# Kernel tuning notes

Measured on AMD Instinct MI355X. Metric: run time of the kernel, lower is better.

Reference implementation:

```python
import jax, jax.numpy as jnp
import numpy as np

B, S, QD = 1, 2048, 3072          # batch, seq, query_dim
H, D = 24, 128                    # heads, head_dim
INNER = H * D                     # 3072
MLP = 4 * QD                      # mlp_hidden_dim = 12288
EPS = 1e-5


def setup_inputs() -> dict:
    key = jax.random.key(0)
    k0, k1, k2 = jax.random.split(key, 3)
    hidden_states = jax.random.normal(k0, (B, S, QD), dtype=jnp.float32)
    # RoPE tables (non-neox / interleaved), [S, D/2]
    pos = jnp.arange(S, dtype=jnp.float32)
    inv_freq = 1.0 / (10000.0 ** (jnp.arange(0, D, 2, dtype=jnp.float32) / D))
    ang = pos[:, None] * inv_freq[None, :]
    cos, sin = jnp.cos(ang), jnp.sin(ang)
    # learned params
    W_qkv_mlp = jax.random.normal(k1, (QD, 3 * INNER + 2 * MLP), dtype=jnp.float32) * 0.02
    norm_q_w = jnp.ones((D,), dtype=jnp.float32)
    norm_k_w = jnp.ones((D,), dtype=jnp.float32)
    W_out = jax.random.normal(k2, (INNER + MLP, QD), dtype=jnp.float32) * 0.02
    b_out = jnp.zeros((QD,), dtype=jnp.float32)
    return {"hidden_states": hidden_states, "cos": cos, "sin": sin,
            "W_qkv_mlp": W_qkv_mlp, "norm_q_w": norm_q_w, "norm_k_w": norm_k_w,
            "W_out": W_out, "b_out": b_out}


def _rmsnorm(x, w, eps):
    return x * jax.lax.rsqrt(jnp.mean(x * x, axis=-1, keepdims=True) + eps) * w


def _rope_interleaved(x, cos, sin):
    # x: [B,S,H,D]; cos/sin: [S,D/2]; non-neox pairing (x[2i], x[2i+1]); fp32 math
    xf = x.astype(jnp.float32)
    x1, x2 = xf[..., 0::2], xf[..., 1::2]
    c = cos[None, :, None, :]
    s = sin[None, :, None, :]
    r1 = x1 * c - x2 * s
    r2 = x2 * c + x1 * s
    out = jnp.stack([r1, r2], axis=-1).reshape(x.shape)
    return out.astype(x.dtype)


def reference(hidden_states, cos, sin, W_qkv_mlp, norm_q_w, norm_k_w, W_out, b_out):
    # fused QKV + MLP input projection (no bias)
    h = hidden_states @ W_qkv_mlp                       # [B,S,3*INNER+2*MLP]
    qkv, mlp_hidden = jnp.split(h, [3 * INNER], axis=-1)
    q, k, v = jnp.split(qkv, 3, axis=-1)
    q = q.reshape(B, S, H, D)
    k = k.reshape(B, S, H, D)
    v = v.reshape(B, S, H, D)
    # per-head RMSNorm on q/k
    q = _rmsnorm(q, norm_q_w, EPS)
    k = _rmsnorm(k, norm_k_w, EPS)
    # interleaved RoPE
    q = _rope_interleaved(q, cos, sin)
    k = _rope_interleaved(k, cos, sin)
    # non-causal attention, scale = 1/sqrt(head_dim)
    scale = 1.0 / np.sqrt(D).astype(np.float32)
    scores = jnp.einsum('bqhd,bkhd->bhqk', q, k) * scale
    probs = jax.nn.softmax(scores, axis=-1)
    attn_out = jnp.einsum('bhqk,bkhd->bqhd', probs, v).reshape(B, S, INNER)
    # SwiGLU on fused MLP hidden (gate fused into first GEMM)
    x1, x2 = jnp.split(mlp_hidden, 2, axis=-1)
    mlp_out = jax.nn.silu(x1) * x2                      # [B,S,MLP]
    # fused output projection (with bias)
    return jnp.concatenate([attn_out, mlp_out], axis=-1) @ W_out + b_out
```

## Files before the change

kernel.cpp:

```cpp
#include <hip/hip_runtime.h>

typedef unsigned short u16;
typedef unsigned int u32;
typedef __attribute__((ext_vector_type(8))) __bf16 bf16x8;
typedef __attribute__((ext_vector_type(4))) float f32x4;
typedef __attribute__((ext_vector_type(8))) u16 u16x8;
typedef __attribute__((ext_vector_type(4))) float fv4;

#define DEVI __device__ __forceinline__

DEVI float bf2f(u16 u) { union { u32 i; float f; } v; v.i = ((u32)u) << 16; return v.f; }
DEVI u16 f2bf(float f) {
  union { float f; u32 i; } v; v.f = f;
  u32 r = v.i + 0x7fffu + ((v.i >> 16) & 1u);
  return (u16)(r >> 16);
}

#define GLD16(src, dst)                                                        \
  __builtin_amdgcn_global_load_lds(                                            \
      (const __attribute__((address_space(1))) void*)(src),                    \
      (__attribute__((address_space(3))) void*)(dst), 16, 0, 0)

DEVI f32x4 mfma16(bf16x8 a, bf16x8 b, f32x4 c) {
  return __builtin_amdgcn_mfma_f32_16x16x32_bf16(a, b, c, 0, 0, 0);
}

constexpr int S_    = 2048;
constexpr int QD_   = 3072;
constexpr int H_    = 24;
constexpr int N1_   = 33792;
constexpr int K1_   = 3072;
constexpr int K2_   = 15360;
constexpr int N2_   = 3072;
constexpr int MLP_  = 12288;

__global__ void k_cvt(const float* __restrict__ in, u16* __restrict__ out) {
  int i = blockIdx.x * blockDim.x + threadIdx.x;
  const fv4* p = (const fv4*)in + (size_t)i * 2;
  fv4 a = p[0], b = p[1];
  u16x8 r;
#pragma unroll
  for (int e = 0; e < 4; ++e) { r[e] = f2bf(a[e]); r[4 + e] = f2bf(b[e]); }
  ((u16x8*)out)[i] = r;
}

__global__ __launch_bounds__(256)
void k_tconv(const float* __restrict__ in, u16* __restrict__ out, int R, int C) {
  __shared__ u16 tile[64][80];
  const int t = threadIdx.x;
  const int r0 = blockIdx.y * 64, c0 = blockIdx.x * 64;
  {
    const int rl = t >> 2, cc = t & 3;
    const float* src = in + (size_t)(r0 + rl) * C + c0 + cc * 16;
    fv4 v0 = *(const fv4*)(src), v1 = *(const fv4*)(src + 4);
    fv4 v2 = *(const fv4*)(src + 8), v3 = *(const fv4*)(src + 12);
    u16x8 u0, u1;
#pragma unroll
    for (int e = 0; e < 4; ++e) {
      u0[e] = f2bf(v0[e]); u0[4 + e] = f2bf(v1[e]);
      u1[e] = f2bf(v2[e]); u1[4 + e] = f2bf(v3[e]);
    }
    *(u16x8*)&tile[rl][cc * 16] = u0;
    *(u16x8*)&tile[rl][cc * 16 + 8] = u1;
  }
  __syncthreads();
  {
    const int cl = t >> 2, rc = t & 3;
    u16x8 u0, u1;
#pragma unroll
    for (int j = 0; j < 8; ++j) {
      u0[j] = tile[rc * 16 + j][cl];
      u1[j] = tile[rc * 16 + 8 + j][cl];
    }
    u16* dst = out + (size_t)(c0 + cl) * R + r0 + rc * 16;
    *(u16x8*)dst = u0;
    *(u16x8*)(dst + 8) = u1;
  }
}

template <int BM, int BN, int WM, int WN, bool OUTF32>
__global__ __launch_bounds__(256)
void k_gemm(const u16* __restrict__ A, const u16* __restrict__ Bt,
            void* __restrict__ Cout, const float* __restrict__ bias,
            int M, int N, int K) {
  constexpr int FM = WM / 16, FN = WN / 16;
  constexpr int WNC = BN / WN;
  __shared__ u16 As[BM * 32];
  __shared__ u16 Bs[BN * 32];
  const int t = threadIdx.x, w = t >> 6, lane = t & 63;
  const int m0 = blockIdx.x * BM, n0 = blockIdx.y * BN;
  const int wr = w / WNC, wc = w % WNC;
  const int g = lane >> 4, rr = lane & 15;
  const int sm = lane >> 2, sk = (lane & 3) * 8;
  f32x4 acc[FM][FN] = {};
  const int nk = K >> 5;
  for (int kt = 0; kt < nk; ++kt) {
    __syncthreads();
    const int kb = kt * 32 + sk;
#pragma unroll
    for (int c = 0; c < BM / 64; ++c) {
      const int ch = w + c * 4;
      GLD16(A + (size_t)(m0 + ch * 16 + sm) * K + kb, &As[ch * 512]);
    }
#pragma unroll
    for (int c = 0; c < BN / 64; ++c) {
      const int ch = w + c * 4;
      GLD16(Bt + (size_t)(n0 + ch * 16 + sm) * K + kb, &Bs[ch * 512]);
    }
    __syncthreads();
    bf16x8 af[FM], bfr[FN];
#pragma unroll
    for (int mi = 0; mi < FM; ++mi)
      af[mi] = *reinterpret_cast<const bf16x8*>(&As[(wr * WM + mi * 16 + rr) * 32 + g * 8]);
#pragma unroll
    for (int ni = 0; ni < FN; ++ni)
      bfr[ni] = *reinterpret_cast<const bf16x8*>(&Bs[(wc * WN + ni * 16 + rr) * 32 + g * 8]);
#pragma unroll
    for (int mi = 0; mi < FM; ++mi)
#pragma unroll
      for (int ni = 0; ni < FN; ++ni)
        acc[mi][ni] = mfma16(af[mi], bfr[ni], acc[mi][ni]);
  }
#pragma unroll
  for (int mi = 0; mi < FM; ++mi)
#pragma unroll
    for (int ni = 0; ni < FN; ++ni) {
      const int row = m0 + wr * WM + mi * 16 + g * 4;
      const int col = n0 + wc * WN + ni * 16 + rr;
#pragma unroll
      for (int j = 0; j < 4; ++j) {
        if constexpr (OUTF32)
          ((float*)Cout)[(size_t)(row + j) * N + col] = acc[mi][ni][j] + bias[col];
        else
          ((u16*)Cout)[(size_t)(row + j) * N + col] = f2bf(acc[mi][ni][j]);
      }
    }
}

#define BARX() asm volatile("s_barrier" ::: "memory")
__global__ __launch_bounds__(512, 2)
void k_gemm256(const u16* __restrict__ A, const u16* __restrict__ Bt,
               u16* __restrict__ C, int N, int K, int nbm) {
  extern __shared__ char smem[];
  const int t = threadIdx.x;
  const int w = t >> 6, lane = t & 63;
  const int wr = w >> 2, wc = w & 3, bh = wc >> 1;
  const int g = lane >> 4, rr = lane & 15;
  const int nwg = gridDim.x, bid = blockIdx.x;
  const int swz = (bid & 7) * (nwg >> 3) + (bid >> 3);
  const int m0 = (swz % nbm) * 256;
  const int n0 = (swz / nbm) * 256;
  const int o = t * 16;
  const int ou = o ^ (((o >> 9) & 1) << 5);
  const int srow = ((ou >> 10) >> 1) * 16 + ((ou >> 6) & 15);
  const int scol = ((ou >> 10) & 1) * 32 + ((ou & 63) >> 1);
  const int soff = (rr * 64 + g * 16) ^ (((rr >> 3) & 1) << 5);
  const int bnoff = (wc & 1) * 8192;
  const int nk = K >> 6;

  const u16* Arow = A + (size_t)(m0 + srow) * K + scol;
  const u16* Brow = Bt + (size_t)(n0 + srow) * K + scol;
#define LDSA(buf, h) (smem + ((buf) * 2 + (h)) * 16384 + w * 1024)
#define LDSB(buf, h) (smem + 65536 + ((buf) * 2 + (h)) * 16384 + w * 1024)
#define STG(rowptr, h, k0, dst)                                   \
  do {                                                            \
    const u16* _s = (rowptr) + (size_t)(h) * 128 * K + (k0);      \
    GLD16(_s, (dst));                                             \
    GLD16(_s + (size_t)64 * K, (dst) + 8192);                     \
  } while (0)

  STG(Arow, 0, 0, LDSA(0, 0));
  STG(Arow, 1, 0, LDSA(0, 1));
  STG(Brow, 0, 0, LDSB(0, 0));
  STG(Brow, 1, 0, LDSB(0, 1));
  STG(Brow, 0, 64, LDSB(1, 0));
  STG(Brow, 1, 64, LDSB(1, 1));
  STG(Arow, 0, 64, LDSA(1, 0));
  asm volatile("s_waitcnt vmcnt(6)" ::: "memory");
  BARX();

  f32x4 acc[8][4] = {};
  for (int j = 0; j < nk; ++j) {
    const int b = j & 1;
    const char* Ab = smem + ((b << 1) + wr) * 16384;
    const char* Bb = smem + 65536 + ((b << 1) + bh) * 16384;
    const int jb = (j + 2 < nk) ? j + 2 : nk - 1;
    bf16x8 aL[4][2], aH[4][2], bL[2][2], bH[2][2];
#pragma unroll
    for (int m = 0; m < 4; ++m)
#pragma unroll
      for (int kk = 0; kk < 2; ++kk)
        aL[m][kk] = *(const bf16x8*)(Ab + m * 2048 + kk * 1024 + soff);
#pragma unroll
    for (int n = 0; n < 2; ++n)
#pragma unroll
      for (int kk = 0; kk < 2; ++kk)
        bL[n][kk] = *(const bf16x8*)(Bb + bnoff + n * 2048 + kk * 1024 + soff);
    if (j + 1 < nk) STG(Arow, 1, (j + 1) * 64, LDSA((j + 1) & 1, 1));
    BARX();
    __builtin_amdgcn_s_setprio(1);
#pragma unroll
    for (int m = 0; m < 4; ++m)
#pragma unroll
      for (int n = 0; n < 2; ++n)
#pragma unroll
        for (int kk = 0; kk < 2; ++kk)
          acc[m][n] = mfma16(aL[m][kk], bL[n][kk], acc[m][n]);
    __builtin_amdgcn_s_setprio(0);
    BARX();
#pragma unroll
    for (int n = 0; n < 2; ++n)
#pragma unroll
      for (int kk = 0; kk < 2; ++kk)
        bH[n][kk] = *(const bf16x8*)(Bb + bnoff + (n + 2) * 2048 + kk * 1024 + soff);
    BARX();
    __builtin_amdgcn_s_setprio(1);
#pragma unroll
    for (int m = 0; m < 4; ++m)
#pragma unroll
      for (int n = 0; n < 2; ++n)
#pragma unroll
        for (int kk = 0; kk < 2; ++kk)
          acc[m][n + 2] = mfma16(aL[m][kk], bH[n][kk], acc[m][n + 2]);
    __builtin_amdgcn_s_setprio(0);
    BARX();
#pragma unroll
    for (int m = 0; m < 4; ++m)
#pragma unroll
      for (int kk = 0; kk < 2; ++kk)
        aH[m][kk] = *(const bf16x8*)(Ab + (m + 4) * 2048 + kk * 1024 + soff);
    STG(Brow, 0, jb * 64, LDSB(b, 0));
    BARX();
    __builtin_amdgcn_s_setprio(1);
#pragma unroll
    for (int m = 0; m < 4; ++m)
#pragma unroll
      for (int n = 0; n < 2; ++n)
#pragma unroll
        for (int kk = 0; kk < 2; ++kk)
          acc[m + 4][n] = mfma16(aH[m][kk], bL[n][kk], acc[m + 4][n]);
    __builtin_amdgcn_s_setprio(0);
    BARX();
    STG(Brow, 1, jb * 64, LDSB(b, 1));
    STG(Arow, 0, jb * 64, LDSA(b, 0));
    asm volatile("s_waitcnt vmcnt(6)" ::: "memory");
    BARX();
    __builtin_amdgcn_s_setprio(1);
#pragma unroll
    for (int m = 0; m < 4; ++m)
#pragma unroll
      for (int n = 0; n < 2; ++n)
#pragma unroll
        for (int kk = 0; kk < 2; ++kk)
          acc[m + 4][n + 2] = mfma16(aH[m][kk], bH[n][kk], acc[m + 4][n + 2]);
    __builtin_amdgcn_s_setprio(0);
    BARX();
  }
#pragma unroll
  for (int m = 0; m < 8; ++m)
#pragma unroll
    for (int n = 0; n < 4; ++n) {
      const int row = m0 + wr * 128 + m * 16 + g * 4;
      const int col = n0 + wc * 64 + n * 16 + rr;
#pragma unroll
      for (int jj = 0; jj < 4; ++jj)
        C[(size_t)(row + jj) * N + col] = f2bf(acc[m][n][jj]);
    }
#undef LDSA
#undef LDSB
#undef STG
}

__global__ __launch_bounds__(256)
void k_qknr(u16* __restrict__ h, const float* __restrict__ cosT,
            const float* __restrict__ sinT, const float* __restrict__ wq,
            const float* __restrict__ wk) {
  const int row = blockIdx.x * 4 + (threadIdx.x >> 6);
  const int lane = threadIdx.x & 63;
  const int s = row / 48;
  const int r2 = row - s * 48;
  const int qk = r2 / 24;
  const int head = r2 - qk * 24;
  u16* base = h + (size_t)s * N1_ + qk * 3072 + head * 128;
  u32 pv = *(const u32*)(base + 2 * lane);
  float x1 = bf2f((u16)(pv & 0xffff)), x2 = bf2f((u16)(pv >> 16));
  float ss = x1 * x1 + x2 * x2;
#pragma unroll
  for (int off = 32; off >= 1; off >>= 1) ss += __shfl_xor(ss, off);
  const float inv = rsqrtf(ss * (1.0f / 128.0f) + 1e-5f);
  const float* wv = qk ? wk : wq;
  const float w1 = wv[2 * lane], w2 = wv[2 * lane + 1];
  const float c = cosT[s * 64 + lane], sn = sinT[s * 64 + lane];
  float xn1 = x1 * inv * w1, xn2 = x2 * inv * w2;
  float r1 = xn1 * c - xn2 * sn;
  float r2v = xn2 * c + xn1 * sn;
  if (!qk) { r1 *= 0.08838834764831845f; r2v *= 0.08838834764831845f; }
  *(u32*)(base + 2 * lane) = (u32)f2bf(r1) | ((u32)f2bf(r2v) << 16);
}

__global__ __launch_bounds__(256)
void k_vt(const u16* __restrict__ h, u16* __restrict__ vt) {
  __shared__ u16 tile[64][144];
  const int t = threadIdx.x;
  const int head = blockIdx.y;
  const int s0 = blockIdx.x * 64;
  {
    const int sl = t >> 2, cc = t & 3;
    const u16* src = h + (size_t)(s0 + sl) * N1_ + 6144 + head * 128 + cc * 32;
#pragma unroll
    for (int q = 0; q < 4; ++q)
      *(u16x8*)&tile[sl][cc * 32 + q * 8] = *(const u16x8*)(src + q * 8);
  }
  __syncthreads();
  {
    const int d = t & 127, half = t >> 7;
    u16* dst = vt + ((size_t)head * 128 + d) * S_ + s0 + half * 32;
#pragma unroll
    for (int q = 0; q < 4; ++q) {
      u16x8 v;
#pragma unroll
      for (int e = 0; e < 8; ++e) v[e] = tile[half * 32 + q * 8 + e][d];
      *(u16x8*)(dst + q * 8) = v;
    }
  }
}

__global__ __launch_bounds__(256)
void k_attn(const u16* __restrict__ h, const u16* __restrict__ vt,
            u16* __restrict__ cc) {
  extern __shared__ char smem[];
  char* KsB = smem;
  char* VsB = smem + 32768;
  const int t = threadIdx.x, w = t >> 6, lane = t & 63;
  const int g = lane >> 4, c = lane & 15;
  u16* Pw = (u16*)(smem + 65536 + w * 2304);
  const int head = blockIdx.y;
  const int q0 = blockIdx.x * 64 + w * 16;
  const int wb = w * 1024;

  const u16* ksrc[4];
  const u16* vsrc[4];
#pragma unroll
  for (int p = 0; p < 4; ++p) {
    const int o = p * 4096 + wb + lane * 16;
    {
      const int kc = o >> 12, r = (o >> 6) & 63, db = o & 63;
      ksrc[p] = h + (size_t)r * N1_ + 3072 + head * 128 + kc * 32 + db / 2;
    }
    {
      const int ks = o >> 13, d = (o >> 6) & 127, db = o & 63;
      vsrc[p] = vt + (size_t)(head * 128 + d) * S_ + ks * 32 + db / 2;
    }
  }
#define STAGEA(ts, buf)                                                     \
  do {                                                                      \
    const size_t _ka = (size_t)(ts) * 64 * N1_;                             \
    const int _kv = (ts) * 64;                                              \
    _Pragma("unroll") for (int p = 0; p < 4; ++p)                           \
        GLD16(ksrc[p] + _ka, KsB + (buf) * 16384 + p * 4096 + wb);          \
    _Pragma("unroll") for (int p = 0; p < 4; ++p)                           \
        GLD16(vsrc[p] + _kv, VsB + (buf) * 16384 + p * 4096 + wb);          \
  } while (0)

  bf16x8 aq[4];
  {
    const u16* qr = h + (size_t)(q0 + c) * N1_ + head * 128;
#pragma unroll
    for (int kc = 0; kc < 4; ++kc)
      aq[kc] = *reinterpret_cast<const bf16x8*>(qr + kc * 32 + g * 8);
  }
  f32x4 o[8] = {};
  float m_[4] = {-1e30f, -1e30f, -1e30f, -1e30f};
  float l_[4] = {0.f, 0.f, 0.f, 0.f};

  STAGEA(0, 0);
  STAGEA(1, 1);
  asm volatile("s_waitcnt vmcnt(8)" ::: "memory");
  __builtin_amdgcn_s_barrier();

  for (int tt = 0; tt < 32; ++tt) {
    const int buf = tt & 1;
    const char* Kb = KsB + buf * 16384;
    const char* Vb = VsB + buf * 16384;
    f32x4 sc[4] = {};
    __builtin_amdgcn_s_setprio(1);
#pragma unroll
    for (int nf = 0; nf < 4; ++nf)
#pragma unroll
      for (int kc = 0; kc < 4; ++kc) {
        bf16x8 bk = *(const bf16x8*)(Kb + kc * 4096 + (nf * 16 + c) * 64 + g * 16);
        sc[nf] = mfma16(aq[kc], bk, sc[nf]);
      }
    __builtin_amdgcn_s_setprio(0);
    float rmax[4];
#pragma unroll
    for (int j = 0; j < 4; ++j)
      rmax[j] = fmaxf(fmaxf(sc[0][j], sc[1][j]), fmaxf(sc[2][j], sc[3][j]));
#pragma unroll
    for (int j = 0; j < 4; ++j)
#pragma unroll
      for (int off = 8; off >= 1; off >>= 1)
        rmax[j] = fmaxf(rmax[j], __shfl_xor(rmax[j], off));
    float al[4], rs[4];
#pragma unroll
    for (int j = 0; j < 4; ++j) {
      const float mn = fmaxf(m_[j], rmax[j]);
      al[j] = __expf(m_[j] - mn);
      m_[j] = mn;
      rs[j] = 0.f;
    }
#pragma unroll
    for (int nf = 0; nf < 4; ++nf)
#pragma unroll
      for (int j = 0; j < 4; ++j) {
        const float pr = __expf(sc[nf][j] - m_[j]);
        sc[nf][j] = pr;
        rs[j] += pr;
      }
#pragma unroll
    for (int j = 0; j < 4; ++j) {
#pragma unroll
      for (int off = 8; off >= 1; off >>= 1) rs[j] += __shfl_xor(rs[j], off);
      l_[j] = l_[j] * al[j] + rs[j];
    }
#pragma unroll
    for (int of = 0; of < 8; ++of)
#pragma unroll
      for (int j = 0; j < 4; ++j) o[of][j] *= al[j];
#pragma unroll
    for (int nf = 0; nf < 4; ++nf)
#pragma unroll
      for (int j = 0; j < 4; ++j)
        Pw[(g * 4 + j) * 72 + nf * 16 + c] = f2bf(sc[nf][j]);
    asm volatile("s_waitcnt lgkmcnt(0)" ::: "memory");
    bf16x8 ap[2];
#pragma unroll
    for (int ks = 0; ks < 2; ++ks)
      ap[ks] = *(const bf16x8*)(Pw + c * 72 + ks * 32 + g * 8);
    __builtin_amdgcn_s_setprio(1);
#pragma unroll
    for (int of = 0; of < 8; ++of)
#pragma unroll
      for (int ks = 0; ks < 2; ++ks) {
        bf16x8 bv = *(const bf16x8*)(Vb + ks * 8192 + (of * 16 + c) * 64 + g * 16);
        o[of] = mfma16(ap[ks], bv, o[of]);
      }
    __builtin_amdgcn_s_setprio(0);
    __builtin_amdgcn_s_barrier();
    const int tn = (tt + 2 < 32) ? tt + 2 : 31;
    STAGEA(tn, buf);
    asm volatile("s_waitcnt vmcnt(8)" ::: "memory");
    __builtin_amdgcn_s_barrier();
  }
  float inv[4];
#pragma unroll
  for (int j = 0; j < 4; ++j) inv[j] = 1.0f / l_[j];
#pragma unroll
  for (int of = 0; of < 8; ++of)
#pragma unroll
    for (int j = 0; j < 4; ++j)
      cc[(size_t)(q0 + g * 4 + j) * K2_ + head * 128 + of * 16 + c] =
          f2bf(o[of][j] * inv[j]);
#undef STAGEA
}

__global__ void k_mlpact(const u16* __restrict__ h, u16* __restrict__ cc) {
  const int i = blockIdx.x * blockDim.x + threadIdx.x;
  const int s = i / 1536;
  const int j8 = i - s * 1536;
  const u16x8 a8 = *((const u16x8*)(h + (size_t)s * N1_ + 9216) + j8);
  const u16x8 b8 = *((const u16x8*)(h + (size_t)s * N1_ + 21504) + j8);
  u16x8 r;
#pragma unroll
  for (int e = 0; e < 8; ++e) {
    float a = bf2f(a8[e]), b = bf2f(b8[e]);
    float sv = a / (1.0f + expf(-a));
    r[e] = f2bf(sv * b);
  }
  *((u16x8*)(cc + (size_t)s * K2_ + 3072) + j8) = r;
}

extern "C" void kernel_launch(void* const* d_in, const int* in_sizes, int n_in,
                              void* d_out, int out_size, void* d_ws,
                              size_t ws_size, hipStream_t stream) {
  const float* hs   = (const float*)d_in[0];
  const float* cosT = (const float*)d_in[1];
  const float* sinT = (const float*)d_in[2];
  const float* W1   = (const float*)d_in[3];
  const float* wq   = (const float*)d_in[4];
  const float* wk   = (const float*)d_in[5];
  const float* W2   = (const float*)d_in[6];
  const float* bo   = (const float*)d_in[7];
  float* out = (float*)d_out;

  char* p = (char*)d_ws;
  u16* Abf  = (u16*)p; p += (size_t)S_ * K1_ * 2;
  u16* W1t  = (u16*)p; p += (size_t)N1_ * K1_ * 2;
  u16* W2t  = (u16*)p; p += (size_t)N2_ * K2_ * 2;
  u16* Hbuf = (u16*)p; p += (size_t)S_ * N1_ * 2;
  u16* Vt   = (u16*)p; p += (size_t)H_ * 128 * S_ * 2;
  u16* CC   = (u16*)p; p += (size_t)S_ * K2_ * 2;
  if ((size_t)(p - (char*)d_ws) > ws_size) return;

  k_cvt<<<(S_ * K1_) / (256 * 8), 256, 0, stream>>>(hs, Abf);
  k_tconv<<<dim3(N1_ / 64, K1_ / 64), 256, 0, stream>>>(W1, W1t, K1_, N1_);
  k_tconv<<<dim3(N2_ / 64, K2_ / 64), 256, 0, stream>>>(W2, W2t, K2_, N2_);

  hipError_t aerr = hipFuncSetAttribute(
      reinterpret_cast<const void*>(k_gemm256),
      hipFuncAttributeMaxDynamicSharedMemorySize, 131072);
  if (aerr == hipSuccess) {
    k_gemm256<<<dim3(1056), 512, 131072, stream>>>(Abf, W1t, Hbuf,
                                                   N1_, K1_, 8);
  } else {
    k_gemm<128, 128, 64, 64, false>
        <<<dim3(S_ / 128, N1_ / 128), 256, 0, stream>>>(Abf, W1t, Hbuf, nullptr,
                                                        S_, N1_, K1_);
  }
  k_qknr<<<(S_ * 2 * H_) / 4, 256, 0, stream>>>(Hbuf, cosT, sinT, wq, wk);
  k_vt<<<dim3(S_ / 64, H_), 256, 0, stream>>>(Hbuf, Vt);
  (void)hipFuncSetAttribute(reinterpret_cast<const void*>(k_attn),
                            hipFuncAttributeMaxDynamicSharedMemorySize, 75776);
  k_attn<<<dim3(S_ / 64, H_), 256, 75776, stream>>>(Hbuf, Vt, CC);
  k_mlpact<<<(S_ * MLP_) / (256 * 8), 256, 0, stream>>>(Hbuf, CC);
  k_gemm<128, 128, 64, 64, true>
      <<<dim3(S_ / 128, N2_ / 128), 256, 0, stream>>>(CC, W2t, out, bo,
                                                      S_, N2_, K2_);
}
```

Before: 1.223 ms.

## Transpose weights via register 8x8 blocks and add explicit LDS waitcnts in GEMM

Replaces the LDS-tiled fp32-to-bf16 weight transpose with a register-only version in which each thread loads an 8x8 fp32 block and writes eight 16-byte bf16 rows, with 128x128 tiles per block. This removes the shared-memory staging and barrier and widens the output writes. The global reads become strided 32-byte row segments, which may coalesce less well. The main GEMM also gets explicit lgkmcnt waits around its barriers, so the LDS fragment loads partly overlap the barrier instead of relying on compiler-inserted waits.

```diff
diff --git a/kernel.cpp b/kernel.cpp
--- a/kernel.cpp
+++ b/kernel.cpp
@@ -45,36 +45,27 @@
 }
 
 __global__ __launch_bounds__(256)
-void k_tconv(const float* __restrict__ in, u16* __restrict__ out, int R, int C) {
-  __shared__ u16 tile[64][80];
+void k_tconv8(const float* __restrict__ in, u16* __restrict__ out,
+              int R, int C) {
   const int t = threadIdx.x;
-  const int r0 = blockIdx.y * 64, c0 = blockIdx.x * 64;
-  {
-    const int rl = t >> 2, cc = t & 3;
-    const float* src = in + (size_t)(r0 + rl) * C + c0 + cc * 16;
-    fv4 v0 = *(const fv4*)(src), v1 = *(const fv4*)(src + 4);
-    fv4 v2 = *(const fv4*)(src + 8), v3 = *(const fv4*)(src + 12);
-    u16x8 u0, u1;
-#pragma unroll
-    for (int e = 0; e < 4; ++e) {
-      u0[e] = f2bf(v0[e]); u0[4 + e] = f2bf(v1[e]);
-      u1[e] = f2bf(v2[e]); u1[4 + e] = f2bf(v3[e]);
-    }
-    *(u16x8*)&tile[rl][cc * 16] = u0;
-    *(u16x8*)&tile[rl][cc * 16 + 8] = u1;
-  }
-  __syncthreads();
-  {
-    const int cl = t >> 2, rc = t & 3;
-    u16x8 u0, u1;
-#pragma unroll
-    for (int j = 0; j < 8; ++j) {
-      u0[j] = tile[rc * 16 + j][cl];
-      u1[j] = tile[rc * 16 + 8 + j][cl];
-    }
-    u16* dst = out + (size_t)(c0 + cl) * R + r0 + rc * 16;
-    *(u16x8*)dst = u0;
-    *(u16x8*)(dst + 8) = u1;
+  const int R8 = t & 15, C8 = t >> 4;
+  const int r0 = blockIdx.y * 128, c0 = blockIdx.x * 128;
+  const float* src = in + (size_t)(r0 + R8 * 8) * C + c0 + C8 * 8;
+  float rf[8][8];
+#pragma unroll
+  for (int r = 0; r < 8; ++r) {
+    fv4 a = *(const fv4*)(src + (size_t)r * C);
+    fv4 b = *(const fv4*)(src + (size_t)r * C + 4);
+#pragma unroll
+    for (int e = 0; e < 4; ++e) { rf[r][e] = a[e]; rf[r][4 + e] = b[e]; }
+  }
+  u16* dst = out + (size_t)(c0 + C8 * 8) * R + r0 + R8 * 8;
+#pragma unroll
+  for (int i = 0; i < 8; ++i) {
+    u16x8 v;
+#pragma unroll
+    for (int j = 0; j < 8; ++j) v[j] = f2bf(rf[j][i]);
+    *(u16x8*)(dst + (size_t)i * R) = v;
   }
 }
 
@@ -138,6 +129,7 @@
 }
 
 #define BARX() asm volatile("s_barrier" ::: "memory")
+#define LGKM0() asm volatile("s_waitcnt lgkmcnt(0)" ::: "memory")
 __global__ __launch_bounds__(512, 2)
 void k_gemm256(const u16* __restrict__ A, const u16* __restrict__ Bt,
                u16* __restrict__ C, int N, int K, int nbm) {
@@ -197,7 +189,9 @@
       for (int kk = 0; kk < 2; ++kk)
         bL[n][kk] = *(const bf16x8*)(Bb + bnoff + n * 2048 + kk * 1024 + soff);
     if (j + 1 < nk) STG(Arow, 1, (j + 1) * 64, LDSA((j + 1) & 1, 1));
-    BARX();
+    asm volatile("s_waitcnt lgkmcnt(8)" ::: "memory");
+    BARX();
+    LGKM0();
     __builtin_amdgcn_s_setprio(1);
 #pragma unroll
     for (int m = 0; m < 4; ++m)
@@ -214,6 +208,7 @@
       for (int kk = 0; kk < 2; ++kk)
         bH[n][kk] = *(const bf16x8*)(Bb + bnoff + (n + 2) * 2048 + kk * 1024 + soff);
     BARX();
+    LGKM0();
     __builtin_amdgcn_s_setprio(1);
 #pragma unroll
     for (int m = 0; m < 4; ++m)
@@ -231,6 +226,7 @@
         aH[m][kk] = *(const bf16x8*)(Ab + (m + 4) * 2048 + kk * 1024 + soff);
     STG(Brow, 0, jb * 64, LDSB(b, 0));
     BARX();
+    LGKM0();
     __builtin_amdgcn_s_setprio(1);
 #pragma unroll
     for (int m = 0; m < 4; ++m)
@@ -245,6 +241,7 @@
     STG(Arow, 0, jb * 64, LDSA(b, 0));
     asm volatile("s_waitcnt vmcnt(6)" ::: "memory");
     BARX();
+    LGKM0();
     __builtin_amdgcn_s_setprio(1);
 #pragma unroll
     for (int m = 0; m < 4; ++m)
@@ -503,8 +500,8 @@
   if ((size_t)(p - (char*)d_ws) > ws_size) return;
 
   k_cvt<<<(S_ * K1_) / (256 * 8), 256, 0, stream>>>(hs, Abf);
-  k_tconv<<<dim3(N1_ / 64, K1_ / 64), 256, 0, stream>>>(W1, W1t, K1_, N1_);
-  k_tconv<<<dim3(N2_ / 64, K2_ / 64), 256, 0, stream>>>(W2, W2t, K2_, N2_);
+  k_tconv8<<<dim3(N1_ / 128, K1_ / 128), 256, 0, stream>>>(W1, W1t, K1_, N1_);
+  k_tconv8<<<dim3(N2_ / 128, K2_ / 128), 256, 0, stream>>>(W2, W2t, K2_, N2_);
 
   hipError_t aerr = hipFuncSetAttribute(
       reinterpret_cast<const void*>(k_gemm256),
```

Result: no change. 1.238 ms (+1.3%).
